# Performance work log

Hardware: AMD Instinct MI355X
Metric: run time of the kernel (lower is better)

Reference implementation:

```python
import jax, jax.numpy as jnp
import numpy as np

B, NQ, NK, D_IN, HD = 1, 16384, 7933, 1024, 512
R = 0.3  # keep-top-r fraction used for the quantile threshold


def _l2norm(x):
    # matches F.normalize(p=2, dim=-1, eps=1e-12)
    n = jnp.linalg.norm(x, axis=-1, keepdims=True)
    return x / jnp.maximum(n, 1e-12)


def setup_inputs() -> dict:
    key = jax.random.key(0)
    ks = jax.random.split(key, 10)
    s = 0.02
    return {
        "query": jax.random.normal(ks[0], (B, NQ, D_IN), jnp.float32),
        "key_x": jax.random.normal(ks[1], (B, NK, D_IN), jnp.float32),
        "wq_w": jax.random.normal(ks[2], (HD, D_IN), jnp.float32) * s,
        "wq_b": jnp.zeros((HD,), jnp.float32),
        "wk_w": jax.random.normal(ks[3], (HD, D_IN), jnp.float32) * s,
        "wk_b": jnp.zeros((HD,), jnp.float32),
        "wa_w": jax.random.normal(ks[4], (1, NK), jnp.float32) * s,
        "wa_b": jnp.zeros((1,), jnp.float32),
        "cls_w": jax.random.normal(ks[5], (1, HD), jnp.float32) * s,
        "cls_b": jnp.zeros((1,), jnp.float32),
    }


def reference(query, key_x, wq_w, wq_b, wk_w, wk_b, wa_w, wa_b, cls_w, cls_b):
    # WQ / WK: Linear + Tanh
    q = jnp.tanh(jnp.einsum("bnd,hd->bnh", query, wq_w) + wq_b)   # [B,NQ,HD]
    k = jnp.tanh(jnp.einsum("bnd,hd->bnh", key_x, wk_w) + wk_b)   # [B,NK,HD]
    # normalized dot-product scores
    A = jnp.einsum("bqh,bkh->bqk", _l2norm(q), _l2norm(k))        # [B,NQ,NK]
    # WA: Linear(NK -> 1)
    A1 = jnp.einsum("bqk,ok->bqo", A, wa_w) + wa_b                # [B,NQ,1]
    # quantile threshold from batch 0 (torch: sorted ascending, index -int(r*NQ))
    thre = jax.lax.stop_gradient(jnp.sort(A1[0, :, 0])[-int(R * NQ)])
    A1 = jnp.where(A1 > thre, A1, 0.0)                            # F.threshold(., thre, 0)
    attn = jax.nn.softmax(A1, axis=1)                             # softmax over NQ (zeros included)
    attn_t = jnp.transpose(attn, (0, 2, 1))                       # [B,1,NQ]
    z = jnp.matmul(attn_t, q).reshape(-1, HD)                     # [B,HD]
    y_prob = z @ cls_w.T + cls_b                                  # [B,1]
    return (y_prob, attn_t)
```

## Files before the change

kernel.cpp:

```cpp
#include <hip/hip_runtime.h>
#include <math.h>

#define NQ 16384
#define NK 7933
#define DI 1024
#define HD 512
#define RANK_TARGET 11469

typedef __bf16 bf16x8 __attribute__((ext_vector_type(8)));
typedef float  f32x4  __attribute__((ext_vector_type(4)));

#define GLOAD_LDS16(g, l)                                                     \
  __builtin_amdgcn_global_load_lds(                                           \
      (const __attribute__((address_space(1))) void*)(g),                     \
      (__attribute__((address_space(3))) void*)(l), 16, 0, 0)

__device__ __forceinline__ unsigned mapf(float f) {
  unsigned b = __float_as_uint(f);
  return (b & 0x80000000u) ? ~b : (b | 0x80000000u);
}

__device__ __forceinline__ bf16x8 cvt8(float4 a, float4 b) {
  bf16x8 o;
  o[0] = (__bf16)a.x; o[1] = (__bf16)a.y; o[2] = (__bf16)a.z; o[3] = (__bf16)a.w;
  o[4] = (__bf16)b.x; o[5] = (__bf16)b.y; o[6] = (__bf16)b.z; o[7] = (__bf16)b.w;
  return o;
}

__global__ void conv_wk(const float* __restrict__ wq, const float* __restrict__ wk,
                        const float* __restrict__ key,
                        __bf16* __restrict__ wqbf, __bf16* __restrict__ wkbf,
                        __bf16* __restrict__ kbf, unsigned* __restrict__ zero_region,
                        uint2* __restrict__ a1zero) {
  if (blockIdx.x == 0) {
    for (int j = threadIdx.x; j < 1088; j += 256) zero_region[j] = 0u;
  } else if (blockIdx.x < 65) {
    int g = (blockIdx.x - 1) * 256 + threadIdx.x;
    uint2 zz; zz.x = 0u; zz.y = 0u;
    a1zero[g] = zz;
  }
  const int NK8 = NK * DI / 8;
  const int W8  = HD * DI / 8;
  const int total = NK8 + 2 * W8;
  int i = blockIdx.x * blockDim.x + threadIdx.x;
  int stride = gridDim.x * blockDim.x;
  for (; i < total; i += stride) {
    const float* s; __bf16* d; int j;
    if (i < NK8)            { s = key; d = kbf;  j = i; }
    else if (i < NK8 + W8)  { s = wq;  d = wqbf; j = i - NK8; }
    else                    { s = wk;  d = wkbf; j = i - NK8 - W8; }
    float4 a = ((const float4*)s)[2 * j];
    float4 b = ((const float4*)s)[2 * j + 1];
    ((bf16x8*)d)[j] = cvt8(a, b);
  }
}

template <bool FUSE_A1>
__device__ __forceinline__ void gemm_core(
    const __bf16* __restrict__ A, const __bf16* __restrict__ B,
    const float* __restrict__ bias, float* __restrict__ C, int M,
    int m0, int n0, __bf16* sA, __bf16* sB,
    const float* __restrict__ v, float* __restrict__ A1dot,
    float* __restrict__ A1ss) {
  constexpr int K = DI;
  constexpr int N = HD;
  const int tid  = threadIdx.x;
  const int lane = tid & 63;
  const int wave = tid >> 6;
  const int wr = wave >> 2;
  const int wc = wave & 3;

  const int srow = lane >> 3;
  const int scol = ((lane & 7) ^ srow) << 3;
  const int lrow = lane & 15;
  const int chi  = lane >> 4;

  int gaA = m0 + wave * 8 + srow; if (gaA > M - 1) gaA = M - 1;
  const __bf16* Ap  = A + (size_t)gaA * K + scol;
  const __bf16* Bp0 = B + (size_t)(n0 + (wave * 4 + 0) * 8 + srow) * K + scol;
  const __bf16* Bp1 = B + (size_t)(n0 + (wave * 4 + 1) * 8 + srow) * K + scol;
  const __bf16* Bp2 = B + (size_t)(n0 + (wave * 4 + 2) * 8 + srow) * K + scol;
  const __bf16* Bp3 = B + (size_t)(n0 + (wave * 4 + 3) * 8 + srow) * K + scol;

  f32x4 acc[2][4] = {};

  GLOAD_LDS16(Ap,  &sA[wave * 512]);
  GLOAD_LDS16(Bp0, &sB[(wave * 4 + 0) * 512]);
  GLOAD_LDS16(Bp1, &sB[(wave * 4 + 1) * 512]);
  GLOAD_LDS16(Bp2, &sB[(wave * 4 + 2) * 512]);
  GLOAD_LDS16(Bp3, &sB[(wave * 4 + 3) * 512]);
  __syncthreads();

  int buf = 0;
  for (int t = 0; t < 16; ++t) {
    const int kk = t * 64;
    if (t < 15) {
      const int ob = (buf ^ 1);
      GLOAD_LDS16(Ap + kk + 64,  &sA[ob * 4096 + wave * 512]);
      GLOAD_LDS16(Bp0 + kk + 64, &sB[ob * 16384 + (wave * 4 + 0) * 512]);
      GLOAD_LDS16(Bp1 + kk + 64, &sB[ob * 16384 + (wave * 4 + 1) * 512]);
      GLOAD_LDS16(Bp2 + kk + 64, &sB[ob * 16384 + (wave * 4 + 2) * 512]);
      GLOAD_LDS16(Bp3 + kk + 64, &sB[ob * 16384 + (wave * 4 + 3) * 512]);
    }
    const __bf16* sAc = sA + buf * 4096;
    const __bf16* sBc = sB + buf * 16384;
#pragma unroll
    for (int ks = 0; ks < 64; ks += 32) {
      const int cc = (ks >> 3) + chi;
      const int sw = ((cc ^ (lrow & 7)) << 3);
      bf16x8 af[2], bfr[4];
      af[0] = *(const bf16x8*)(&sAc[(wr * 32 + lrow) * 64 + sw]);
      af[1] = *(const bf16x8*)(&sAc[(wr * 32 + 16 + lrow) * 64 + sw]);
#pragma unroll
      for (int ni = 0; ni < 4; ++ni)
        bfr[ni] = *(const bf16x8*)(&sBc[(wc * 64 + ni * 16 + lrow) * 64 + sw]);
#pragma unroll
      for (int ni = 0; ni < 4; ++ni) {
        acc[0][ni] = __builtin_amdgcn_mfma_f32_16x16x32_bf16(af[0], bfr[ni], acc[0][ni], 0, 0, 0);
        acc[1][ni] = __builtin_amdgcn_mfma_f32_16x16x32_bf16(af[1], bfr[ni], acc[1][ni], 0, 0, 0);
      }
    }
    if (t < 15) {
      __syncthreads();
      buf ^= 1;
    }
  }

  const int rbase = m0 + wr * 32 + ((lane >> 4) << 2);
  const int cbase = n0 + wc * 64 + (lane & 15);
  float b4[4], v4[4];
#pragma unroll
  for (int ni = 0; ni < 4; ++ni) {
    b4[ni] = bias[cbase + ni * 16];
    if constexpr (FUSE_A1) v4[ni] = v[cbase + ni * 16];
  }
#pragma unroll
  for (int mi = 0; mi < 2; ++mi) {
#pragma unroll
    for (int r = 0; r < 4; ++r) {
      int grow = rbase + mi * 16 + r;
      if (grow < M) {
        float pd = 0.f, pss = 0.f;
#pragma unroll
        for (int ni = 0; ni < 4; ++ni) {
          float val = tanhf(acc[mi][ni][r] + b4[ni]);
          C[(size_t)grow * N + cbase + ni * 16] = val;
          if constexpr (FUSE_A1) { pd += val * v4[ni]; pss += val * val; }
        }
        if constexpr (FUSE_A1) {
#pragma unroll
          for (int off = 1; off < 16; off <<= 1) {
            pd += __shfl_xor(pd, off);
            pss += __shfl_xor(pss, off);
          }
          if ((lane & 15) == 0) {
            atomicAdd(&A1dot[grow], pd);
            atomicAdd(&A1ss[grow], pss);
          }
        }
      }
    }
  }
}

__global__ __launch_bounds__(512, 4)
void gemm_k_fused(const __bf16* __restrict__ kbf, const __bf16* __restrict__ wkbf,
                  const float* __restrict__ wk_b, const float* __restrict__ wa,
                  float* __restrict__ v,
                  const float* __restrict__ query, __bf16* __restrict__ qbf) {
  __shared__ __align__(16) __bf16 sA[2 * 64 * 64];
  __shared__ __align__(16) __bf16 sB[512 * 64];
  __shared__ float ssrow[64];
  const int bid = blockIdx.x;
  const int tid = threadIdx.x;

  if (bid >= 124) {
    const int total = NQ * DI / 8;
    for (int i = (bid - 124) * 512 + tid; i < total; i += 388 * 512) {
      float4 a = ((const float4*)query)[2 * i];
      float4 b = ((const float4*)query)[2 * i + 1];
      ((bf16x8*)qbf)[i] = cvt8(a, b);
    }
    return;
  }

  constexpr int K = DI;
  const int lane = tid & 63;
  const int wave = tid >> 6;
  const int m0 = bid * 64;

  const int srow = lane >> 3;
  const int scol = ((lane & 7) ^ srow) << 3;
  const int lrow = lane & 15;
  const int chi  = lane >> 4;

  int gaA = m0 + wave * 8 + srow; if (gaA > NK - 1) gaA = NK - 1;
  const __bf16* Ap = kbf + (size_t)gaA * K + scol;
  const __bf16* Bp[8];
#pragma unroll
  for (int c = 0; c < 8; ++c)
    Bp[c] = wkbf + (size_t)(wave * 64 + c * 8 + srow) * K + scol;

  f32x4 acc[4][4] = {};

  GLOAD_LDS16(Ap, &sA[wave * 512]);
#pragma unroll
  for (int c = 0; c < 8; ++c)
    GLOAD_LDS16(Bp[c], &sB[(wave * 8 + c) * 512]);
  __syncthreads();

  int buf = 0;
  for (int t = 0; t < 16; ++t) {
    const int kk = t * 64;
    if (t < 15)
      GLOAD_LDS16(Ap + kk + 64, &sA[(buf ^ 1) * 4096 + wave * 512]);
    const __bf16* sAc = sA + buf * 4096;
#pragma unroll
    for (int ks = 0; ks < 64; ks += 32) {
      const int cc = (ks >> 3) + chi;
      const int sw = ((cc ^ (lrow & 7)) << 3);
      bf16x8 af[4], bfr[4];
#pragma unroll
      for (int mi = 0; mi < 4; ++mi)
        af[mi] = *(const bf16x8*)(&sAc[(mi * 16 + lrow) * 64 + sw]);
#pragma unroll
      for (int ni = 0; ni < 4; ++ni)
        bfr[ni] = *(const bf16x8*)(&sB[(wave * 64 + ni * 16 + lrow) * 64 + sw]);
#pragma unroll
      for (int mi = 0; mi < 4; ++mi)
#pragma unroll
        for (int ni = 0; ni < 4; ++ni)
          acc[mi][ni] = __builtin_amdgcn_mfma_f32_16x16x32_bf16(af[mi], bfr[ni], acc[mi][ni], 0, 0, 0);
    }
    if (t < 15) {
      __syncthreads();
#pragma unroll
      for (int c = 0; c < 8; ++c)
        GLOAD_LDS16(Bp[c] + kk + 64, &sB[(wave * 8 + c) * 512]);
      __syncthreads();
      buf ^= 1;
    }
  }

  __syncthreads();
  if (tid < 64) ssrow[tid] = 0.f;
  __syncthreads();

  float b4[4];
#pragma unroll
  for (int ni = 0; ni < 4; ++ni) b4[ni] = wk_b[wave * 64 + ni * 16 + lrow];

#pragma unroll
  for (int mi = 0; mi < 4; ++mi)
#pragma unroll
    for (int ni = 0; ni < 4; ++ni)
#pragma unroll
      for (int r = 0; r < 4; ++r)
        acc[mi][ni][r] = tanhf(acc[mi][ni][r] + b4[ni]);

#pragma unroll
  for (int mi = 0; mi < 4; ++mi)
#pragma unroll
    for (int r = 0; r < 4; ++r) {
      float ps = 0.f;
#pragma unroll
      for (int ni = 0; ni < 4; ++ni) ps += acc[mi][ni][r] * acc[mi][ni][r];
#pragma unroll
      for (int off = 1; off < 16; off <<= 1) ps += __shfl_xor(ps, off);
      if ((lane & 15) == 0)
        atomicAdd(&ssrow[mi * 16 + (lane >> 4) * 4 + r], ps);
    }
  __syncthreads();

  if (tid < 64) {
    int grow = m0 + tid;
    float s = 0.f;
    if (grow < NK) s = wa[grow] / fmaxf(sqrtf(ssrow[tid]), 1e-12f);
    ssrow[tid] = s;
  }
  __syncthreads();

  float sc[4][4];
#pragma unroll
  for (int mi = 0; mi < 4; ++mi)
#pragma unroll
    for (int r = 0; r < 4; ++r)
      sc[mi][r] = ssrow[mi * 16 + (lane >> 4) * 4 + r];

#pragma unroll
  for (int ni = 0; ni < 4; ++ni) {
    float cs = 0.f;
#pragma unroll
    for (int mi = 0; mi < 4; ++mi)
#pragma unroll
      for (int r = 0; r < 4; ++r)
        cs += acc[mi][ni][r] * sc[mi][r];
    cs += __shfl_xor(cs, 16);
    cs += __shfl_xor(cs, 32);
    if (lane < 16) atomicAdd(&v[wave * 64 + ni * 16 + lane], cs);
  }
}

__global__ __launch_bounds__(512, 4)
void gemm_q(const __bf16* __restrict__ qbf, const __bf16* __restrict__ wqbf,
            const float* __restrict__ wq_b, float* __restrict__ qtanh,
            const float* __restrict__ v, float* __restrict__ A1dot,
            float* __restrict__ A1ss) {
  __shared__ __align__(16) __bf16 sA[2 * 64 * 64];
  __shared__ __align__(16) __bf16 sB[2 * 256 * 64];
  gemm_core<true>(qbf, wqbf, wq_b, qtanh, NQ, blockIdx.x * 64, blockIdx.y * 256,
                  sA, sB, v, A1dot, A1ss);
}

__global__ __launch_bounds__(1024)
void select_kernel(const float* __restrict__ A1dot, const float* __restrict__ A1ss,
                   const float* __restrict__ wa_b, float* __restrict__ A1,
                   float* __restrict__ scf) {
  __shared__ unsigned wred1[16], wred2[16], wred3[16];
  __shared__ unsigned s_res;
  const int t = threadIdx.x, lane = t & 63, wave = t >> 6;
  const float wab = wa_b[0];
  unsigned kloc[16];
#pragma unroll 4
  for (int j = 0; j < 16; ++j) {
    int i = j * 1024 + t;
    float d = A1dot[i], ss = A1ss[i];
    float a1 = d / fmaxf(sqrtf(ss), 1e-12f) + wab;
    A1[i] = a1;
    kloc[j] = mapf(a1);
  }
  if (t == 0) s_res = 0u;
  __syncthreads();

  for (int b = 30; b >= 0; b -= 2) {
    const unsigned res = s_res;
    const unsigned t1 = res | (1u << b);
    const unsigned t2 = res | (2u << b);
    const unsigned t3 = res | (3u << b);
    unsigned c1 = 0, c2 = 0, c3 = 0;
#pragma unroll
    for (int j = 0; j < 16; ++j) {
      unsigned k = kloc[j];
      c1 += (k < t1); c2 += (k < t2); c3 += (k < t3);
    }
#pragma unroll
    for (int off = 32; off; off >>= 1) {
      c1 += __shfl_xor(c1, off);
      c2 += __shfl_xor(c2, off);
      c3 += __shfl_xor(c3, off);
    }
    if (lane == 0) { wred1[wave] = c1; wred2[wave] = c2; wred3[wave] = c3; }
    __syncthreads();
    if (t == 0) {
      unsigned C1 = 0, C2 = 0, C3 = 0;
      for (int w = 0; w < 16; ++w) { C1 += wred1[w]; C2 += wred2[w]; C3 += wred3[w]; }
      unsigned nr = res;
      if (C3 <= RANK_TARGET)      nr = t3;
      else if (C2 <= RANK_TARGET) nr = t2;
      else if (C1 <= RANK_TARGET) nr = t1;
      s_res = nr;
    }
    __syncthreads();
  }
  if (t == 0) {
    unsigned key = s_res;
    unsigned bits = (key & 0x80000000u) ? (key ^ 0x80000000u) : ~key;
    scf[0] = __uint_as_float(bits);
  }
}

__global__ __launch_bounds__(256)
void expz(const float* __restrict__ A1, const float* __restrict__ qt,
          float* __restrict__ scf, float* __restrict__ e_out,
          float* __restrict__ z) {
  __shared__ float vpart[4][512];
  __shared__ float esum[4];
  const int tid = threadIdx.x, lane = tid & 63, wave = tid >> 6;
  const float thre = scf[0];
  const int gw = blockIdx.x * 4 + wave;
  const int tw = gridDim.x * 4;
  float acc[8] = {0, 0, 0, 0, 0, 0, 0, 0};
  float es = 0.f;
  for (int r = gw; r < NQ; r += tw) {
    float x = A1[r]; x = (x > thre) ? x : 0.f;
    float e = expf(x - thre);
    if (lane == 0) e_out[r] = e;
    es += e;
    const float4* p = (const float4*)(qt + (size_t)r * HD + lane * 8);
    float4 u = p[0], w = p[1];
    acc[0] += e * u.x; acc[1] += e * u.y; acc[2] += e * u.z; acc[3] += e * u.w;
    acc[4] += e * w.x; acc[5] += e * w.y; acc[6] += e * w.z; acc[7] += e * w.w;
  }
  if (lane == 0) esum[wave] = es;
#pragma unroll
  for (int j = 0; j < 8; ++j) vpart[wave][lane * 8 + j] = acc[j];
  __syncthreads();
  for (int c = tid; c < 512; c += 256)
    atomicAdd(&z[c], vpart[0][c] + vpart[1][c] + vpart[2][c] + vpart[3][c]);
  if (tid == 0) atomicAdd(&scf[2], esum[0] + esum[1] + esum[2] + esum[3]);
}

__global__ __launch_bounds__(256)
void finalize(float* __restrict__ attn, const float* __restrict__ scf,
              const float* __restrict__ z, const float* __restrict__ cls_w,
              const float* __restrict__ cls_b, float* __restrict__ y) {
  const float invZ = 1.f / scf[2];
  if (blockIdx.x < 64) {
    int i = blockIdx.x * 256 + threadIdx.x;
    attn[i] *= invZ;
  } else if (threadIdx.x < 64) {
    const int lane = threadIdx.x;
    const float4* zp = (const float4*)(z + lane * 8);
    const float4* wp = (const float4*)(cls_w + lane * 8);
    float4 a = zp[0], b = zp[1], c = wp[0], d = wp[1];
    float dot = a.x * c.x + a.y * c.y + a.z * c.z + a.w * c.w
              + b.x * d.x + b.y * d.y + b.z * d.z + b.w * d.w;
#pragma unroll
    for (int off = 32; off; off >>= 1) dot += __shfl_xor(dot, off);
    if (lane == 0) y[0] = dot * invZ + cls_b[0];
  }
}

#define OFF_WQBF 0u
#define OFF_WKBF 1048576u
#define OFF_QBF  2097152u
#define OFF_A1   35651584u
#define OFF_V    35717120u
#define OFF_Z    35719168u
#define OFF_SC   35721216u
#define OFF_KBF  35721472u
#define OFF_QT   52428800u
#define OFF_A1D  88080384u
#define OFF_A1S  88145920u

extern "C" void kernel_launch(void* const* d_in, const int* in_sizes, int n_in,
                              void* d_out, int out_size, void* d_ws, size_t ws_size,
                              hipStream_t stream) {
  const float* query = (const float*)d_in[0];
  const float* key_x = (const float*)d_in[1];
  const float* wq_w  = (const float*)d_in[2];
  const float* wq_b  = (const float*)d_in[3];
  const float* wk_w  = (const float*)d_in[4];
  const float* wk_b  = (const float*)d_in[5];
  const float* wa_w  = (const float*)d_in[6];
  const float* wa_b  = (const float*)d_in[7];
  const float* cls_w = (const float*)d_in[8];
  const float* cls_b = (const float*)d_in[9];
  float* out = (float*)d_out;

  char* ws = (char*)d_ws;
  __bf16* wqbf  = (__bf16*)(ws + OFF_WQBF);
  __bf16* wkbf  = (__bf16*)(ws + OFF_WKBF);
  __bf16* qbf   = (__bf16*)(ws + OFF_QBF);
  float*  A1    = (float*)(ws + OFF_A1);
  float*  v     = (float*)(ws + OFF_V);
  float*  z     = (float*)(ws + OFF_Z);
  float*  scf   = (float*)(ws + OFF_SC);
  __bf16* kbf   = (__bf16*)(ws + OFF_KBF);
  float*  qtanh = (float*)(ws + OFF_QT);
  float*  A1dot = (float*)(ws + OFF_A1D);
  float*  A1ss  = (float*)(ws + OFF_A1S);
  float*  out_attn = out + 1;

  conv_wk<<<2048, 256, 0, stream>>>(wq_w, wk_w, key_x, wqbf, wkbf, kbf,
                                    (unsigned*)v, (uint2*)A1dot);

  gemm_k_fused<<<512, 512, 0, stream>>>(kbf, wkbf, wk_b, wa_w, v, query, qbf);

  gemm_q<<<dim3(256, 2), 512, 0, stream>>>(qbf, wqbf, wq_b, qtanh, v, A1dot, A1ss);

  select_kernel<<<1, 1024, 0, stream>>>(A1dot, A1ss, wa_b, A1, scf);

  expz<<<256, 256, 0, stream>>>(A1, qtanh, scf, out_attn, z);

  finalize<<<65, 256, 0, stream>>>(out_attn, scf, z, cls_w, cls_b, out);
}
```

Measured before the change: 250.8 us.

## Merge K and Q GEMMs into one launch with in-kernel fp32→bf16 query conversion

The K-side GEMM and the Q-side GEMM now run as independent block ranges of a single kernel. The Q GEMM reads fp32 query directly and converts it to bf16 while staging into LDS, so the separate qbf buffer and its write/read round trip go away. Because v is no longer finished when the Q GEMM runs, the A1 dot product and norm move into a new a1_pass kernel that rereads qtanh. This also removes the per-row atomics. The cost is an extra 32 MB read of qtanh and register-staged A loads in the Q path, which may be less efficient than direct global-to-LDS loads.

```diff
diff --git a/kernel.cpp b/kernel.cpp
--- a/kernel.cpp
+++ b/kernel.cpp
@@ -30,14 +30,9 @@
 __global__ void conv_wk(const float* __restrict__ wq, const float* __restrict__ wk,
                         const float* __restrict__ key,
                         __bf16* __restrict__ wqbf, __bf16* __restrict__ wkbf,
-                        __bf16* __restrict__ kbf, unsigned* __restrict__ zero_region,
-                        uint2* __restrict__ a1zero) {
+                        __bf16* __restrict__ kbf, unsigned* __restrict__ zero_region) {
   if (blockIdx.x == 0) {
     for (int j = threadIdx.x; j < 1088; j += 256) zero_region[j] = 0u;
-  } else if (blockIdx.x < 65) {
-    int g = (blockIdx.x - 1) * 256 + threadIdx.x;
-    uint2 zz; zz.x = 0u; zz.y = 0u;
-    a1zero[g] = zz;
   }
   const int NK8 = NK * DI / 8;
   const int W8  = HD * DI / 8;
@@ -55,280 +50,254 @@
   }
 }
 
-template <bool FUSE_A1>
-__device__ __forceinline__ void gemm_core(
-    const __bf16* __restrict__ A, const __bf16* __restrict__ B,
-    const float* __restrict__ bias, float* __restrict__ C, int M,
-    int m0, int n0, __bf16* sA, __bf16* sB,
-    const float* __restrict__ v, float* __restrict__ A1dot,
-    float* __restrict__ A1ss) {
-  constexpr int K = DI;
-  constexpr int N = HD;
-  const int tid  = threadIdx.x;
+__global__ __launch_bounds__(512, 4)
+void mega_gemms(const __bf16* __restrict__ kbf, const __bf16* __restrict__ wkbf,
+                const float* __restrict__ wk_b, const float* __restrict__ wa,
+                float* __restrict__ v,
+                const float* __restrict__ query, const __bf16* __restrict__ wqbf,
+                const float* __restrict__ wq_b, float* __restrict__ qtanh) {
+  __shared__ __align__(16) char smem[81920];
+  const int bid = blockIdx.x;
+  const int tid = threadIdx.x;
   const int lane = tid & 63;
   const int wave = tid >> 6;
-  const int wr = wave >> 2;
-  const int wc = wave & 3;
-
   const int srow = lane >> 3;
   const int scol = ((lane & 7) ^ srow) << 3;
   const int lrow = lane & 15;
   const int chi  = lane >> 4;
-
-  int gaA = m0 + wave * 8 + srow; if (gaA > M - 1) gaA = M - 1;
-  const __bf16* Ap  = A + (size_t)gaA * K + scol;
-  const __bf16* Bp0 = B + (size_t)(n0 + (wave * 4 + 0) * 8 + srow) * K + scol;
-  const __bf16* Bp1 = B + (size_t)(n0 + (wave * 4 + 1) * 8 + srow) * K + scol;
-  const __bf16* Bp2 = B + (size_t)(n0 + (wave * 4 + 2) * 8 + srow) * K + scol;
-  const __bf16* Bp3 = B + (size_t)(n0 + (wave * 4 + 3) * 8 + srow) * K + scol;
-
-  f32x4 acc[2][4] = {};
-
-  GLOAD_LDS16(Ap,  &sA[wave * 512]);
-  GLOAD_LDS16(Bp0, &sB[(wave * 4 + 0) * 512]);
-  GLOAD_LDS16(Bp1, &sB[(wave * 4 + 1) * 512]);
-  GLOAD_LDS16(Bp2, &sB[(wave * 4 + 2) * 512]);
-  GLOAD_LDS16(Bp3, &sB[(wave * 4 + 3) * 512]);
-  __syncthreads();
-
-  int buf = 0;
-  for (int t = 0; t < 16; ++t) {
-    const int kk = t * 64;
-    if (t < 15) {
-      const int ob = (buf ^ 1);
-      GLOAD_LDS16(Ap + kk + 64,  &sA[ob * 4096 + wave * 512]);
-      GLOAD_LDS16(Bp0 + kk + 64, &sB[ob * 16384 + (wave * 4 + 0) * 512]);
-      GLOAD_LDS16(Bp1 + kk + 64, &sB[ob * 16384 + (wave * 4 + 1) * 512]);
-      GLOAD_LDS16(Bp2 + kk + 64, &sB[ob * 16384 + (wave * 4 + 2) * 512]);
-      GLOAD_LDS16(Bp3 + kk + 64, &sB[ob * 16384 + (wave * 4 + 3) * 512]);
-    }
-    const __bf16* sAc = sA + buf * 4096;
-    const __bf16* sBc = sB + buf * 16384;
-#pragma unroll
-    for (int ks = 0; ks < 64; ks += 32) {
-      const int cc = (ks >> 3) + chi;
-      const int sw = ((cc ^ (lrow & 7)) << 3);
-      bf16x8 af[2], bfr[4];
-      af[0] = *(const bf16x8*)(&sAc[(wr * 32 + lrow) * 64 + sw]);
-      af[1] = *(const bf16x8*)(&sAc[(wr * 32 + 16 + lrow) * 64 + sw]);
+  constexpr int K = DI;
+
+  if (bid < 124) {
+    __bf16* sA = (__bf16*)smem;
+    __bf16* sB = (__bf16*)(smem + 16384);
+    float* ssrow = (float*)smem;
+    const int m0 = bid * 64;
+
+    int gaA = m0 + wave * 8 + srow; if (gaA > NK - 1) gaA = NK - 1;
+    const __bf16* Ap = kbf + (size_t)gaA * K + scol;
+    const __bf16* Bp[8];
+#pragma unroll
+    for (int c = 0; c < 8; ++c)
+      Bp[c] = wkbf + (size_t)(wave * 64 + c * 8 + srow) * K + scol;
+
+    f32x4 acc[4][4] = {};
+
+    GLOAD_LDS16(Ap, &sA[wave * 512]);
+#pragma unroll
+    for (int c = 0; c < 8; ++c)
+      GLOAD_LDS16(Bp[c], &sB[(wave * 8 + c) * 512]);
+    __syncthreads();
+
+    int buf = 0;
+    for (int t = 0; t < 16; ++t) {
+      const int kk = t * 64;
+      if (t < 15)
+        GLOAD_LDS16(Ap + kk + 64, &sA[(buf ^ 1) * 4096 + wave * 512]);
+      const __bf16* sAc = sA + buf * 4096;
+#pragma unroll
+      for (int ks = 0; ks < 64; ks += 32) {
+        const int cc = (ks >> 3) + chi;
+        const int sw = ((cc ^ (lrow & 7)) << 3);
+        bf16x8 af[4], bfr[4];
+#pragma unroll
+        for (int mi = 0; mi < 4; ++mi)
+          af[mi] = *(const bf16x8*)(&sAc[(mi * 16 + lrow) * 64 + sw]);
+#pragma unroll
+        for (int ni = 0; ni < 4; ++ni)
+          bfr[ni] = *(const bf16x8*)(&sB[(wave * 64 + ni * 16 + lrow) * 64 + sw]);
+#pragma unroll
+        for (int mi = 0; mi < 4; ++mi)
+#pragma unroll
+          for (int ni = 0; ni < 4; ++ni)
+            acc[mi][ni] = __builtin_amdgcn_mfma_f32_16x16x32_bf16(af[mi], bfr[ni], acc[mi][ni], 0, 0, 0);
+      }
+      if (t < 15) {
+        __syncthreads();
+#pragma unroll
+        for (int c = 0; c < 8; ++c)
+          GLOAD_LDS16(Bp[c] + kk + 64, &sB[(wave * 8 + c) * 512]);
+        __syncthreads();
+        buf ^= 1;
+      }
+    }
+
+    __syncthreads();
+    if (tid < 64) ssrow[tid] = 0.f;
+    __syncthreads();
+
+    float b4[4];
+#pragma unroll
+    for (int ni = 0; ni < 4; ++ni) b4[ni] = wk_b[wave * 64 + ni * 16 + lrow];
+
+#pragma unroll
+    for (int mi = 0; mi < 4; ++mi)
 #pragma unroll
       for (int ni = 0; ni < 4; ++ni)
-        bfr[ni] = *(const bf16x8*)(&sBc[(wc * 64 + ni * 16 + lrow) * 64 + sw]);
-#pragma unroll
-      for (int ni = 0; ni < 4; ++ni) {
-        acc[0][ni] = __builtin_amdgcn_mfma_f32_16x16x32_bf16(af[0], bfr[ni], acc[0][ni], 0, 0, 0);
-        acc[1][ni] = __builtin_amdgcn_mfma_f32_16x16x32_bf16(af[1], bfr[ni], acc[1][ni], 0, 0, 0);
-      }
-    }
-    if (t < 15) {
+#pragma unroll
+        for (int r = 0; r < 4; ++r)
+          acc[mi][ni][r] = tanhf(acc[mi][ni][r] + b4[ni]);
+
+#pragma unroll
+    for (int mi = 0; mi < 4; ++mi)
+#pragma unroll
+      for (int r = 0; r < 4; ++r) {
+        float ps = 0.f;
+#pragma unroll
+        for (int ni = 0; ni < 4; ++ni) ps += acc[mi][ni][r] * acc[mi][ni][r];
+#pragma unroll
+        for (int off = 1; off < 16; off <<= 1) ps += __shfl_xor(ps, off);
+        if ((lane & 15) == 0)
+          atomicAdd(&ssrow[mi * 16 + (lane >> 4) * 4 + r], ps);
+      }
+    __syncthreads();
+
+    if (tid < 64) {
+      int grow = m0 + tid;
+      float s = 0.f;
+      if (grow < NK) s = wa[grow] / fmaxf(sqrtf(ssrow[tid]), 1e-12f);
+      ssrow[tid] = s;
+    }
+    __syncthreads();
+
+    float sc[4][4];
+#pragma unroll
+    for (int mi = 0; mi < 4; ++mi)
+#pragma unroll
+      for (int r = 0; r < 4; ++r)
+        sc[mi][r] = ssrow[mi * 16 + (lane >> 4) * 4 + r];
+
+#pragma unroll
+    for (int ni = 0; ni < 4; ++ni) {
+      float cs = 0.f;
+#pragma unroll
+      for (int mi = 0; mi < 4; ++mi)
+#pragma unroll
+        for (int r = 0; r < 4; ++r)
+          cs += acc[mi][ni][r] * sc[mi][r];
+      cs += __shfl_xor(cs, 16);
+      cs += __shfl_xor(cs, 32);
+      if (lane < 16) atomicAdd(&v[wave * 64 + ni * 16 + lane], cs);
+    }
+  } else {
+    __bf16* sA = (__bf16*)smem;
+    __bf16* sB = (__bf16*)(smem + 16384);
+    const int qi = bid - 124;
+    const int m0 = (qi >> 1) * 64;
+    const int n0 = (qi & 1) * 256;
+    const int wr = wave >> 2;
+    const int wc = wave & 3;
+
+    const int arow = tid >> 3;
+    const int acb  = tid & 7;
+    const int aoff = arow * 64 + ((acb ^ (arow & 7)) << 3);
+    const float* ap = query + (size_t)(m0 + arow) * K + acb * 8;
+
+    const __bf16* Bp0 = wqbf + (size_t)(n0 + (wave * 4 + 0) * 8 + srow) * K + scol;
+    const __bf16* Bp1 = wqbf + (size_t)(n0 + (wave * 4 + 1) * 8 + srow) * K + scol;
+    const __bf16* Bp2 = wqbf + (size_t)(n0 + (wave * 4 + 2) * 8 + srow) * K + scol;
+    const __bf16* Bp3 = wqbf + (size_t)(n0 + (wave * 4 + 3) * 8 + srow) * K + scol;
+
+    f32x4 acc[2][4] = {};
+
+    {
+      float4 x0 = *(const float4*)(ap);
+      float4 x1 = *(const float4*)(ap + 4);
+      GLOAD_LDS16(Bp0, &sB[(wave * 4 + 0) * 512]);
+      GLOAD_LDS16(Bp1, &sB[(wave * 4 + 1) * 512]);
+      GLOAD_LDS16(Bp2, &sB[(wave * 4 + 2) * 512]);
+      GLOAD_LDS16(Bp3, &sB[(wave * 4 + 3) * 512]);
+      *(bf16x8*)&sA[aoff] = cvt8(x0, x1);
       __syncthreads();
-      buf ^= 1;
-    }
-  }
-
-  const int rbase = m0 + wr * 32 + ((lane >> 4) << 2);
-  const int cbase = n0 + wc * 64 + (lane & 15);
-  float b4[4], v4[4];
-#pragma unroll
-  for (int ni = 0; ni < 4; ++ni) {
-    b4[ni] = bias[cbase + ni * 16];
-    if constexpr (FUSE_A1) v4[ni] = v[cbase + ni * 16];
-  }
-#pragma unroll
-  for (int mi = 0; mi < 2; ++mi) {
-#pragma unroll
-    for (int r = 0; r < 4; ++r) {
-      int grow = rbase + mi * 16 + r;
-      if (grow < M) {
-        float pd = 0.f, pss = 0.f;
+    }
+
+    int buf = 0;
+    for (int t = 0; t < 16; ++t) {
+      const int kk = t * 64;
+      float4 x0, x1;
+      if (t < 15) {
+        x0 = *(const float4*)(ap + kk + 64);
+        x1 = *(const float4*)(ap + kk + 68);
+        const int ob = buf ^ 1;
+        GLOAD_LDS16(Bp0 + kk + 64, &sB[ob * 16384 + (wave * 4 + 0) * 512]);
+        GLOAD_LDS16(Bp1 + kk + 64, &sB[ob * 16384 + (wave * 4 + 1) * 512]);
+        GLOAD_LDS16(Bp2 + kk + 64, &sB[ob * 16384 + (wave * 4 + 2) * 512]);
+        GLOAD_LDS16(Bp3 + kk + 64, &sB[ob * 16384 + (wave * 4 + 3) * 512]);
+      }
+      const __bf16* sAc = sA + buf * 4096;
+      const __bf16* sBc = sB + buf * 16384;
+#pragma unroll
+      for (int ks = 0; ks < 64; ks += 32) {
+        const int cc = (ks >> 3) + chi;
+        const int sw = ((cc ^ (lrow & 7)) << 3);
+        bf16x8 af[2], bfr[4];
+        af[0] = *(const bf16x8*)(&sAc[(wr * 32 + lrow) * 64 + sw]);
+        af[1] = *(const bf16x8*)(&sAc[(wr * 32 + 16 + lrow) * 64 + sw]);
+#pragma unroll
+        for (int ni = 0; ni < 4; ++ni)
+          bfr[ni] = *(const bf16x8*)(&sBc[(wc * 64 + ni * 16 + lrow) * 64 + sw]);
 #pragma unroll
         for (int ni = 0; ni < 4; ++ni) {
-          float val = tanhf(acc[mi][ni][r] + b4[ni]);
-          C[(size_t)grow * N + cbase + ni * 16] = val;
-          if constexpr (FUSE_A1) { pd += val * v4[ni]; pss += val * val; }
+          acc[0][ni] = __builtin_amdgcn_mfma_f32_16x16x32_bf16(af[0], bfr[ni], acc[0][ni], 0, 0, 0);
+          acc[1][ni] = __builtin_amdgcn_mfma_f32_16x16x32_bf16(af[1], bfr[ni], acc[1][ni], 0, 0, 0);
         }
-        if constexpr (FUSE_A1) {
-#pragma unroll
-          for (int off = 1; off < 16; off <<= 1) {
-            pd += __shfl_xor(pd, off);
-            pss += __shfl_xor(pss, off);
-          }
-          if ((lane & 15) == 0) {
-            atomicAdd(&A1dot[grow], pd);
-            atomicAdd(&A1ss[grow], pss);
-          }
-        }
-      }
-    }
-  }
-}
-
-__global__ __launch_bounds__(512, 4)
-void gemm_k_fused(const __bf16* __restrict__ kbf, const __bf16* __restrict__ wkbf,
-                  const float* __restrict__ wk_b, const float* __restrict__ wa,
-                  float* __restrict__ v,
-                  const float* __restrict__ query, __bf16* __restrict__ qbf) {
-  __shared__ __align__(16) __bf16 sA[2 * 64 * 64];
-  __shared__ __align__(16) __bf16 sB[512 * 64];
-  __shared__ float ssrow[64];
-  const int bid = blockIdx.x;
-  const int tid = threadIdx.x;
-
-  if (bid >= 124) {
-    const int total = NQ * DI / 8;
-    for (int i = (bid - 124) * 512 + tid; i < total; i += 388 * 512) {
-      float4 a = ((const float4*)query)[2 * i];
-      float4 b = ((const float4*)query)[2 * i + 1];
-      ((bf16x8*)qbf)[i] = cvt8(a, b);
-    }
-    return;
-  }
-
-  constexpr int K = DI;
-  const int lane = tid & 63;
-  const int wave = tid >> 6;
-  const int m0 = bid * 64;
-
-  const int srow = lane >> 3;
-  const int scol = ((lane & 7) ^ srow) << 3;
-  const int lrow = lane & 15;
-  const int chi  = lane >> 4;
-
-  int gaA = m0 + wave * 8 + srow; if (gaA > NK - 1) gaA = NK - 1;
-  const __bf16* Ap = kbf + (size_t)gaA * K + scol;
-  const __bf16* Bp[8];
-#pragma unroll
-  for (int c = 0; c < 8; ++c)
-    Bp[c] = wkbf + (size_t)(wave * 64 + c * 8 + srow) * K + scol;
-
-  f32x4 acc[4][4] = {};
-
-  GLOAD_LDS16(Ap, &sA[wave * 512]);
-#pragma unroll
-  for (int c = 0; c < 8; ++c)
-    GLOAD_LDS16(Bp[c], &sB[(wave * 8 + c) * 512]);
-  __syncthreads();
-
-  int buf = 0;
-  for (int t = 0; t < 16; ++t) {
-    const int kk = t * 64;
-    if (t < 15)
-      GLOAD_LDS16(Ap + kk + 64, &sA[(buf ^ 1) * 4096 + wave * 512]);
-    const __bf16* sAc = sA + buf * 4096;
-#pragma unroll
-    for (int ks = 0; ks < 64; ks += 32) {
-      const int cc = (ks >> 3) + chi;
-      const int sw = ((cc ^ (lrow & 7)) << 3);
-      bf16x8 af[4], bfr[4];
-#pragma unroll
-      for (int mi = 0; mi < 4; ++mi)
-        af[mi] = *(const bf16x8*)(&sAc[(mi * 16 + lrow) * 64 + sw]);
-#pragma unroll
-      for (int ni = 0; ni < 4; ++ni)
-        bfr[ni] = *(const bf16x8*)(&sB[(wave * 64 + ni * 16 + lrow) * 64 + sw]);
-#pragma unroll
-      for (int mi = 0; mi < 4; ++mi)
+      }
+      if (t < 15) {
+        *(bf16x8*)&sA[(buf ^ 1) * 4096 + aoff] = cvt8(x0, x1);
+        __syncthreads();
+        buf ^= 1;
+      }
+    }
+
+    const int rbase = m0 + wr * 32 + ((lane >> 4) << 2);
+    const int cbase = n0 + wc * 64 + (lane & 15);
+    float b4[4];
+#pragma unroll
+    for (int ni = 0; ni < 4; ++ni) b4[ni] = wq_b[cbase + ni * 16];
+#pragma unroll
+    for (int mi = 0; mi < 2; ++mi)
+#pragma unroll
+      for (int r = 0; r < 4; ++r) {
+        int grow = rbase + mi * 16 + r;
 #pragma unroll
         for (int ni = 0; ni < 4; ++ni)
-          acc[mi][ni] = __builtin_amdgcn_mfma_f32_16x16x32_bf16(af[mi], bfr[ni], acc[mi][ni], 0, 0, 0);
-    }
-    if (t < 15) {
-      __syncthreads();
-#pragma unroll
-      for (int c = 0; c < 8; ++c)
-        GLOAD_LDS16(Bp[c] + kk + 64, &sB[(wave * 8 + c) * 512]);
-      __syncthreads();
-      buf ^= 1;
-    }
-  }
-
-  __syncthreads();
-  if (tid < 64) ssrow[tid] = 0.f;
-  __syncthreads();
-
-  float b4[4];
-#pragma unroll
-  for (int ni = 0; ni < 4; ++ni) b4[ni] = wk_b[wave * 64 + ni * 16 + lrow];
-
-#pragma unroll
-  for (int mi = 0; mi < 4; ++mi)
-#pragma unroll
-    for (int ni = 0; ni < 4; ++ni)
-#pragma unroll
-      for (int r = 0; r < 4; ++r)
-        acc[mi][ni][r] = tanhf(acc[mi][ni][r] + b4[ni]);
-
-#pragma unroll
-  for (int mi = 0; mi < 4; ++mi)
-#pragma unroll
-    for (int r = 0; r < 4; ++r) {
-      float ps = 0.f;
-#pragma unroll
-      for (int ni = 0; ni < 4; ++ni) ps += acc[mi][ni][r] * acc[mi][ni][r];
-#pragma unroll
-      for (int off = 1; off < 16; off <<= 1) ps += __shfl_xor(ps, off);
-      if ((lane & 15) == 0)
-        atomicAdd(&ssrow[mi * 16 + (lane >> 4) * 4 + r], ps);
-    }
-  __syncthreads();
-
-  if (tid < 64) {
-    int grow = m0 + tid;
-    float s = 0.f;
-    if (grow < NK) s = wa[grow] / fmaxf(sqrtf(ssrow[tid]), 1e-12f);
-    ssrow[tid] = s;
-  }
-  __syncthreads();
-
-  float sc[4][4];
-#pragma unroll
-  for (int mi = 0; mi < 4; ++mi)
-#pragma unroll
-    for (int r = 0; r < 4; ++r)
-      sc[mi][r] = ssrow[mi * 16 + (lane >> 4) * 4 + r];
-
-#pragma unroll
-  for (int ni = 0; ni < 4; ++ni) {
-    float cs = 0.f;
-#pragma unroll
-    for (int mi = 0; mi < 4; ++mi)
-#pragma unroll
-      for (int r = 0; r < 4; ++r)
-        cs += acc[mi][ni][r] * sc[mi][r];
-    cs += __shfl_xor(cs, 16);
-    cs += __shfl_xor(cs, 32);
-    if (lane < 16) atomicAdd(&v[wave * 64 + ni * 16 + lane], cs);
-  }
-}
-
-__global__ __launch_bounds__(512, 4)
-void gemm_q(const __bf16* __restrict__ qbf, const __bf16* __restrict__ wqbf,
-            const float* __restrict__ wq_b, float* __restrict__ qtanh,
-            const float* __restrict__ v, float* __restrict__ A1dot,
-            float* __restrict__ A1ss) {
-  __shared__ __align__(16) __bf16 sA[2 * 64 * 64];
-  __shared__ __align__(16) __bf16 sB[2 * 256 * 64];
-  gemm_core<true>(qbf, wqbf, wq_b, qtanh, NQ, blockIdx.x * 64, blockIdx.y * 256,
-                  sA, sB, v, A1dot, A1ss);
+          qtanh[(size_t)grow * HD + cbase + ni * 16] =
+              tanhf(acc[mi][ni][r] + b4[ni]);
+      }
+  }
+}
+
+__global__ __launch_bounds__(256)
+void a1_pass(const float* __restrict__ qt, const float* __restrict__ v,
+             const float* __restrict__ wa_b, float* __restrict__ A1) {
+  const int tid = threadIdx.x, lane = tid & 63, wave = tid >> 6;
+  const float wab = wa_b[0];
+  const float4* vp = (const float4*)(v + lane * 8);
+  float4 vv0 = vp[0], vv1 = vp[1];
+  const int gw = blockIdx.x * 4 + wave;
+  for (int r = gw; r < NQ; r += 2048) {
+    const float4* p = (const float4*)(qt + (size_t)r * HD + lane * 8);
+    float4 u = p[0], w = p[1];
+    float dot = u.x * vv0.x + u.y * vv0.y + u.z * vv0.z + u.w * vv0.w
+              + w.x * vv1.x + w.y * vv1.y + w.z * vv1.z + w.w * vv1.w;
+    float ss  = u.x * u.x + u.y * u.y + u.z * u.z + u.w * u.w
+              + w.x * w.x + w.y * w.y + w.z * w.z + w.w * w.w;
+#pragma unroll
+    for (int off = 32; off; off >>= 1) {
+      dot += __shfl_xor(dot, off);
+      ss  += __shfl_xor(ss, off);
+    }
+    if (lane == 0) A1[r] = dot / fmaxf(sqrtf(ss), 1e-12f) + wab;
+  }
 }
 
 __global__ __launch_bounds__(1024)
-void select_kernel(const float* __restrict__ A1dot, const float* __restrict__ A1ss,
-                   const float* __restrict__ wa_b, float* __restrict__ A1,
-                   float* __restrict__ scf) {
+void select_kernel(const float* __restrict__ A1, float* __restrict__ scf) {
   __shared__ unsigned wred1[16], wred2[16], wred3[16];
   __shared__ unsigned s_res;
   const int t = threadIdx.x, lane = t & 63, wave = t >> 6;
-  const float wab = wa_b[0];
   unsigned kloc[16];
 #pragma unroll 4
-  for (int j = 0; j < 16; ++j) {
-    int i = j * 1024 + t;
-    float d = A1dot[i], ss = A1ss[i];
-    float a1 = d / fmaxf(sqrtf(ss), 1e-12f) + wab;
-    A1[i] = a1;
-    kloc[j] = mapf(a1);
-  }
+  for (int j = 0; j < 16; ++j) kloc[j] = mapf(A1[j * 1024 + t]);
   if (t == 0) s_res = 0u;
   __syncthreads();
 
@@ -423,15 +392,12 @@
 
 #define OFF_WQBF 0u
 #define OFF_WKBF 1048576u
-#define OFF_QBF  2097152u
-#define OFF_A1   35651584u
-#define OFF_V    35717120u
-#define OFF_Z    35719168u
-#define OFF_SC   35721216u
-#define OFF_KBF  35721472u
-#define OFF_QT   52428800u
-#define OFF_A1D  88080384u
-#define OFF_A1S  88145920u
+#define OFF_KBF  2097152u
+#define OFF_QT   18874368u
+#define OFF_A1   52428800u
+#define OFF_V    52494336u
+#define OFF_Z    52496384u
+#define OFF_SC   52498432u
 
 extern "C" void kernel_launch(void* const* d_in, const int* in_sizes, int n_in,
                               void* d_out, int out_size, void* d_ws, size_t ws_size,
@@ -451,25 +417,23 @@
   char* ws = (char*)d_ws;
   __bf16* wqbf  = (__bf16*)(ws + OFF_WQBF);
   __bf16* wkbf  = (__bf16*)(ws + OFF_WKBF);
-  __bf16* qbf   = (__bf16*)(ws + OFF_QBF);
+  __bf16* kbf   = (__bf16*)(ws + OFF_KBF);
+  float*  qtanh = (float*)(ws + OFF_QT);
   float*  A1    = (float*)(ws + OFF_A1);
   float*  v     = (float*)(ws + OFF_V);
   float*  z     = (float*)(ws + OFF_Z);
   float*  scf   = (float*)(ws + OFF_SC);
-  __bf16* kbf   = (__bf16*)(ws + OFF_KBF);
-  float*  qtanh = (float*)(ws + OFF_QT);
-  float*  A1dot = (float*)(ws + OFF_A1D);
-  float*  A1ss  = (float*)(ws + OFF_A1S);
   float*  out_attn = out + 1;
 
   conv_wk<<<2048, 256, 0, stream>>>(wq_w, wk_w, key_x, wqbf, wkbf, kbf,
-                                    (unsigned*)v, (uint2*)A1dot);
-
-  gemm_k_fused<<<512, 512, 0, stream>>>(kbf, wkbf, wk_b, wa_w, v, query, qbf);
-
-  gemm_q<<<dim3(256, 2), 512, 0, stream>>>(qbf, wqbf, wq_b, qtanh, v, A1dot, A1ss);
-
-  select_kernel<<<1, 1024, 0, stream>>>(A1dot, A1ss, wa_b, A1, scf);
+                                    (unsigned*)v);
+
+  mega_gemms<<<636, 512, 0, stream>>>(kbf, wkbf, wk_b, wa_w, v,
+                                      query, wqbf, wq_b, qtanh);
+
+  a1_pass<<<512, 256, 0, stream>>>(qtanh, v, wa_b, A1);
+
+  select_kernel<<<1, 1024, 0, stream>>>(A1, scf);
 
   expz<<<256, 256, 0, stream>>>(A1, qtanh, scf, out_attn, z);
 
```

After: 243.8 us. 2.8% less time.
